# Kernel optimization log

Measured on AMD Instinct MI355X. Metric: run time of the kernel, lower is better.

## Reference

```python
import jax, jax.numpy as jnp
import numpy as np

N, LATENT, HIDDEN, OUT, B = 65536, 128, 512, 64, 1024
W_WIDTH = 4.0  # LSH bucket width params['w']


def setup_inputs() -> dict:
    key = jax.random.key(0)
    ks = jax.random.split(key, 6)
    return {
        "z": jax.random.normal(ks[0], (N, LATENT), jnp.float32),
        "W1": jax.random.normal(ks[1], (LATENT, HIDDEN), jnp.float32) / np.float32(np.sqrt(LATENT)),
        "b1": jnp.zeros((HIDDEN,), jnp.float32),
        "W2": jax.random.normal(ks[2], (HIDDEN, OUT), jnp.float32) / np.float32(np.sqrt(HIDDEN)),
        "b2": jnp.zeros((OUT,), jnp.float32),
        "a": jax.random.normal(ks[3], (OUT,), jnp.float32),
        "lsh_b": jax.random.uniform(ks[4], (1,), jnp.float32) * W_WIDTH,
    }


def reference(z, W1, b1, W2, b2, a, lsh_b):
    # decoder MLP: latent -> hidden (relu) -> output_dim
    h = jax.nn.relu(z @ W1 + b1)
    x = h @ W2 + b2                                     # [N, OUT]
    # LSH random-projection hash: floor((x.a + b)/w), bucketed mod B
    code = jnp.floor((x @ a + lsh_b[0]) / W_WIDTH)
    bucket = jnp.mod(code.astype(jnp.int32), B)         # [N] segment ids
    # dict-based cluster grouping -> segmented mean per hash bucket
    sums = jax.ops.segment_sum(x, bucket, num_segments=B)                # [B, OUT]
    counts = jax.ops.segment_sum(jnp.ones((x.shape[0],), x.dtype), bucket, num_segments=B)
    means = sums / jnp.maximum(counts, 1.0)[:, None]    # [B, OUT]
    # squared distances point -> every cluster mean (gram trick, no [N,B,OUT] tensor)
    d2 = jnp.maximum(
        jnp.sum(x * x, -1)[:, None] + jnp.sum(means * means, -1)[None, :]
        - 2.0 * (x @ means.T),
        0.0)                                            # [N, B]
    # DEC-style Student-t soft cluster assignment
    q = 1.0 / (1.0 + d2)
    q_s = q / jnp.sum(q, -1, keepdims=True)
    return (q_s, means)
```

## Files before the change

### kernel.cpp

```cpp
#include <hip/hip_runtime.h>
#include <hip/hip_bf16.h>

#define N_PTS   65536
#define LATENT  128
#define HIDDEN  512
#define OUT_D   64
#define NBUCKET 1024
#define ROWS_A  32

typedef __attribute__((ext_vector_type(8))) short frag_ab;
typedef __attribute__((ext_vector_type(4))) float f32x4;

__device__ __forceinline__ short bf16h(float f) {
    union { float f; unsigned u; } c; c.f = f;
    const unsigned r = (c.u + 0x7FFFu + ((c.u >> 16) & 1u)) >> 16;
    return (short)r;
}
__device__ __forceinline__ float bf16tof(short s) {
    union { unsigned u; float f; } c; c.u = ((unsigned)(unsigned short)s) << 16;
    return c.f;
}

__global__ __launch_bounds__(256) void prep_weights(
    const float* __restrict__ W1, const float* __restrict__ W2,
    short* __restrict__ w1frag, short* __restrict__ w2frag)
{
    const int tid = blockIdx.x * 256 + threadIdx.x;
    if (tid < 32 * 64 * 4) {
        const int ct = tid >> 8, l = (tid >> 2) & 63, ks = tid & 3;
        const int n = ct * 16 + (l & 15);
        const int k0 = ks * 32 + ((l >> 4) << 3);
        frag_ab hi, lo;
#pragma unroll
        for (int e = 0; e < 8; ++e) {
            const float wv = W1[(size_t)(k0 + e) * HIDDEN + n];
            const short h = bf16h(wv);
            hi[e] = h;
            lo[e] = bf16h(wv - bf16tof(h));
        }
        frag_ab* dst = (frag_ab*)w1frag;
        const int u = ((ct * 64 + l) * 4 + ks) * 2;
        dst[u] = hi; dst[u + 1] = lo;
    } else {
        const int u0 = tid - 32 * 64 * 4;
        const int c = u0 >> 8, ot = (u0 >> 6) & 3, l = u0 & 63;
        const int n = ot * 16 + (l & 15);
        const int k0 = c * 32 + ((l >> 4) << 3);
        frag_ab hi, lo;
#pragma unroll
        for (int e = 0; e < 8; ++e) {
            const float wv = W2[(size_t)(k0 + e) * OUT_D + n];
            const short h = bf16h(wv);
            hi[e] = h;
            lo[e] = bf16h(wv - bf16tof(h));
        }
        frag_ab* dst = (frag_ab*)w2frag;
        const int u = ((c * 4 + ot) * 64 + l) * 2;
        dst[u] = hi; dst[u + 1] = lo;
    }
}

#define WB_UNITS 1728
#define W2_OFF   1152
#define H_OFF    3456
#define HW_UNITS 320
#define XP_STRIDE 512
#define BAND_U   5e-4f

__global__ __launch_bounds__(256, 2) void mlp_mfma_kernel(
    const float* __restrict__ z, const short* __restrict__ w1frag,
    const short* __restrict__ w2frag, const float* __restrict__ b1,
    const float* __restrict__ b2, const float* __restrict__ a,
    const float* __restrict__ lsh_b,
    short* __restrict__ xhi, short* __restrict__ xlo,
    float* __restrict__ xnorm_out, int* __restrict__ bucket_out,
    int* __restrict__ wsflag)
{
    __shared__ frag_ab LD[H_OFF + 4 * HW_UNITS];
    short* LDs = (short*)LD;
    const int t = threadIdx.x;
    const int l = t & 63, w = t >> 6;
    const int row0 = blockIdx.x * 128 + w * 32;

    frag_ab zh[2][4], zl[2][4];
#pragma unroll
    for (int rt = 0; rt < 2; ++rt)
#pragma unroll
        for (int ks = 0; ks < 4; ++ks) {
            const float* src = z + (size_t)(row0 + rt * 16 + (l & 15)) * LATENT
                             + ks * 32 + ((l >> 4) << 3);
            const float4 p0 = *(const float4*)src;
            const float4 p1 = *(const float4*)(src + 4);
            const float v[8] = {p0.x, p0.y, p0.z, p0.w, p1.x, p1.y, p1.z, p1.w};
#pragma unroll
            for (int e = 0; e < 8; ++e) {
                const short h = bf16h(v[e]);
                zh[rt][ks][e] = h;
                zl[rt][ks][e] = bf16h(v[e] - bf16tof(h));
            }
        }

    f32x4 acc2[2][4];
#pragma unroll
    for (int rt = 0; rt < 2; ++rt)
#pragma unroll
        for (int ot = 0; ot < 4; ++ot) acc2[rt][ot] = (f32x4){0.f, 0.f, 0.f, 0.f};

    const frag_ab* w1g = (const frag_ab*)w1frag;
    const frag_ab* w2g = (const frag_ab*)w2frag;
    const int hbase = H_OFF + w * HW_UNITS;

#pragma unroll
    for (int j = 0; j < 4; ++j) {
        const int i = t + 256 * j;
        LD[(i >> 9) * 576 + ((i >> 3) & 63) * 9 + (i & 7)] = w1g[i];
    }
#pragma unroll
    for (int j = 0; j < 2; ++j) {
        const int i = t + 256 * j;
        LD[W2_OFF + ((i >> 1) & 63) * 9 + (((i >> 7) << 1) | (i & 1))] = w2g[i];
    }
    __syncthreads();

#pragma unroll 1
    for (int c = 0; c < 16; ++c) {
        const int pb = (c & 1) * WB_UNITS;
        const int sb = WB_UNITS - pb;
        frag_ab st1[4], st2[2];
        if (c < 15) {
#pragma unroll
            for (int j = 0; j < 4; ++j) st1[j] = w1g[(c + 1) * 1024 + t + 256 * j];
#pragma unroll
            for (int j = 0; j < 2; ++j) st2[j] = w2g[(c + 1) * 512 + t + 256 * j];
        }
#pragma unroll
        for (int ct_l = 0; ct_l < 2; ++ct_l) {
            frag_ab bh[4], bl[4];
#pragma unroll
            for (int ks = 0; ks < 4; ++ks) {
                bh[ks] = LD[pb + ct_l * 576 + l * 9 + ks * 2];
                bl[ks] = LD[pb + ct_l * 576 + l * 9 + ks * 2 + 1];
            }
            const float b1v = b1[(c * 2 + ct_l) * 16 + (l & 15)];
            const int k_l = ct_l * 16 + (l & 15);
            const int gu = k_l >> 3, eu = k_l & 7;
#pragma unroll
            for (int rt = 0; rt < 2; ++rt) {
                f32x4 acc = (f32x4){0.f, 0.f, 0.f, 0.f};
#pragma unroll
                for (int ks = 0; ks < 4; ++ks) {
                    acc = __builtin_amdgcn_mfma_f32_16x16x32_bf16(zh[rt][ks], bh[ks], acc, 0, 0, 0);
                    acc = __builtin_amdgcn_mfma_f32_16x16x32_bf16(zh[rt][ks], bl[ks], acc, 0, 0, 0);
                    acc = __builtin_amdgcn_mfma_f32_16x16x32_bf16(zl[rt][ks], bh[ks], acc, 0, 0, 0);
                }
#pragma unroll
                for (int r = 0; r < 4; ++r) {
                    const float hv = fmaxf(acc[r] + b1v, 0.f);
                    const short hh = bf16h(hv);
                    const short hlo = bf16h(hv - bf16tof(hh));
                    const int row_l = rt * 16 + (l >> 4) * 4 + r;
                    LDs[(hbase + row_l * 5 + gu) * 8 + eu] = hh;
                    LDs[(hbase + 160 + row_l * 5 + gu) * 8 + eu] = hlo;
                }
            }
        }
        frag_ab ah[2], al[2];
#pragma unroll
        for (int rt = 0; rt < 2; ++rt) {
            const int row = rt * 16 + (l & 15);
            const int g = l >> 4;
            ah[rt] = LD[hbase + row * 5 + g];
            al[rt] = LD[hbase + 160 + row * 5 + g];
        }
#pragma unroll
        for (int ot = 0; ot < 4; ++ot) {
            const frag_ab b2h = LD[pb + W2_OFF + l * 9 + ot * 2];
            const frag_ab b2l = LD[pb + W2_OFF + l * 9 + ot * 2 + 1];
#pragma unroll
            for (int rt = 0; rt < 2; ++rt) {
                acc2[rt][ot] = __builtin_amdgcn_mfma_f32_16x16x32_bf16(ah[rt], b2h, acc2[rt][ot], 0, 0, 0);
                acc2[rt][ot] = __builtin_amdgcn_mfma_f32_16x16x32_bf16(ah[rt], b2l, acc2[rt][ot], 0, 0, 0);
                acc2[rt][ot] = __builtin_amdgcn_mfma_f32_16x16x32_bf16(al[rt], b2h, acc2[rt][ot], 0, 0, 0);
            }
        }
        if (c < 15) {
#pragma unroll
            for (int j = 0; j < 4; ++j) {
                const int i = t + 256 * j;
                LD[sb + (i >> 9) * 576 + ((i >> 3) & 63) * 9 + (i & 7)] = st1[j];
            }
#pragma unroll
            for (int j = 0; j < 2; ++j) {
                const int i = t + 256 * j;
                LD[sb + W2_OFF + ((i >> 1) & 63) * 9 + (((i >> 7) << 1) | (i & 1))] = st2[j];
            }
        }
        __syncthreads();
    }

    float b2v[4], av[4];
#pragma unroll
    for (int ot = 0; ot < 4; ++ot) {
        b2v[ot] = b2[ot * 16 + (l & 15)];
        av[ot]  = a[ot * 16 + (l & 15)];
    }
    const int pbase = w * XP_STRIDE;
    int flagged = 0;
    const float lb = lsh_b[0];
#pragma unroll
    for (int rt = 0; rt < 2; ++rt)
#pragma unroll
        for (int r = 0; r < 4; ++r) {
            float sp = 0.f, np = 0.f;
            const int row_l = rt * 16 + (l >> 4) * 4 + r;
#pragma unroll
            for (int ot = 0; ot < 4; ++ot) {
                const float xv = acc2[rt][ot][r] + b2v[ot];
                sp = fmaf(xv, av[ot], sp);
                np = fmaf(xv, xv, np);
                const int col = ot * 16 + (l & 15);
                const short xh = bf16h(xv);
                LDs[(pbase + row_l * 8 + (col >> 3)) * 8 + (col & 7)] = xh;
                LDs[(pbase + 256 + row_l * 8 + (col >> 3)) * 8 + (col & 7)] = bf16h(xv - bf16tof(xh));
            }
#pragma unroll
            for (int off = 8; off >= 1; off >>= 1) {
                sp += __shfl_xor(sp, off, 16);
                np += __shfl_xor(np, off, 16);
            }
            if ((l & 15) == 0) {
                const int row = row0 + row_l;
                const float v = sp + lb;
                const float u = v * 0.25f;
                const float fl = floorf(u);
                bucket_out[row] = ((int)fl) & (NBUCKET - 1);
                xnorm_out[row] = np;
                const float fr = u - fl;
                if (fr < BAND_U || fr > 1.f - BAND_U) flagged = 1;
            }
        }
    const unsigned long long fb = __ballot(flagged != 0);
    if (l == 0) wsflag[blockIdx.x * 4 + w] = (fb != 0ull) ? 1 : 0;

    frag_ab* xhi8 = (frag_ab*)xhi;
    frag_ab* xlo8 = (frag_ab*)xlo;
#pragma unroll
    for (int j = 0; j < 4; ++j) {
        const int u = l + 64 * j;
        const size_t gidx = (size_t)(row0 + (u >> 3)) * 8 + (u & 7);
        xhi8[gidx] = LD[pbase + u];
        xlo8[gidx] = LD[pbase + 256 + u];
    }
}

__global__ __launch_bounds__(256, 3) void mlp_fixup_kernel(
    const float* __restrict__ z, const float* __restrict__ W1,
    const float* __restrict__ b1, const float* __restrict__ W2,
    const float* __restrict__ b2, const float* __restrict__ a,
    const float* __restrict__ lsh_b, const int* __restrict__ wsflag,
    short* __restrict__ xhi, short* __restrict__ xlo,
    float* __restrict__ xnorm_out, int* __restrict__ bucket_out)
{
    if (wsflag[blockIdx.x] == 0) return;
    __shared__ float zt[ROWS_A][LATENT];
    __shared__ float ht[ROWS_A][256];
    const int t = threadIdx.x;
    const int row0 = blockIdx.x * ROWS_A;

    {
        const float4* z4 = reinterpret_cast<const float4*>(z + (size_t)row0 * LATENT);
        float4* zt4 = reinterpret_cast<float4*>(&zt[0][0]);
#pragma unroll
        for (int i = 0; i < 4; ++i) zt4[t + 256 * i] = z4[t + 256 * i];
    }
    __syncthreads();

    const int tx = t & 63, ty = t >> 6;
    const int txq = t & 31, tyq = t >> 5;

    float acc2[4][2];
#pragma unroll
    for (int i = 0; i < 4; ++i) { acc2[i][0] = 0.f; acc2[i][1] = 0.f; }

    for (int h = 0; h < 2; ++h) {
        float acc1[8][4];
#pragma unroll
        for (int i = 0; i < 8; ++i)
#pragma unroll
            for (int cc = 0; cc < 4; ++cc) acc1[i][cc] = 0.f;

        const int jbase = h * 256 + tx;
#pragma unroll 2
        for (int k = 0; k < LATENT; k += 4) {
            float wv[4][4];
#pragma unroll
            for (int kk = 0; kk < 4; ++kk)
#pragma unroll
                for (int cc = 0; cc < 4; ++cc)
                    wv[kk][cc] = W1[(size_t)(k + kk) * HIDDEN + jbase + 64 * cc];
            float4 zv[8];
#pragma unroll
            for (int i = 0; i < 8; ++i)
                zv[i] = *reinterpret_cast<const float4*>(&zt[ty * 8 + i][k]);
#pragma unroll
            for (int i = 0; i < 8; ++i)
#pragma unroll
                for (int cc = 0; cc < 4; ++cc) {
                    acc1[i][cc] = fmaf(zv[i].x, wv[0][cc], acc1[i][cc]);
                    acc1[i][cc] = fmaf(zv[i].y, wv[1][cc], acc1[i][cc]);
                    acc1[i][cc] = fmaf(zv[i].z, wv[2][cc], acc1[i][cc]);
                    acc1[i][cc] = fmaf(zv[i].w, wv[3][cc], acc1[i][cc]);
                }
        }
        float bb[4];
#pragma unroll
        for (int cc = 0; cc < 4; ++cc) bb[cc] = b1[jbase + 64 * cc];
#pragma unroll
        for (int i = 0; i < 8; ++i)
#pragma unroll
            for (int cc = 0; cc < 4; ++cc)
                ht[ty * 8 + i][tx + 64 * cc] = fmaxf(acc1[i][cc] + bb[cc], 0.f);
        __syncthreads();

#pragma unroll 2
        for (int k = 0; k < 256; k += 4) {
            float w2v[4][2];
#pragma unroll
            for (int kk = 0; kk < 4; ++kk) {
                w2v[kk][0] = W2[(size_t)(h * 256 + k + kk) * OUT_D + txq];
                w2v[kk][1] = W2[(size_t)(h * 256 + k + kk) * OUT_D + txq + 32];
            }
            float4 hv[4];
#pragma unroll
            for (int i = 0; i < 4; ++i)
                hv[i] = *reinterpret_cast<const float4*>(&ht[tyq * 4 + i][k]);
#pragma unroll
            for (int i = 0; i < 4; ++i)
#pragma unroll
                for (int cc = 0; cc < 2; ++cc) {
                    acc2[i][cc] = fmaf(hv[i].x, w2v[0][cc], acc2[i][cc]);
                    acc2[i][cc] = fmaf(hv[i].y, w2v[1][cc], acc2[i][cc]);
                    acc2[i][cc] = fmaf(hv[i].z, w2v[2][cc], acc2[i][cc]);
                    acc2[i][cc] = fmaf(hv[i].w, w2v[3][cc], acc2[i][cc]);
                }
        }
        __syncthreads();
    }

    const float bb0 = b2[txq], bb1 = b2[txq + 32];
    const float a0 = a[txq], a1 = a[txq + 32];
    const float lb = lsh_b[0];
#pragma unroll
    for (int i = 0; i < 4; ++i) {
        const int row = row0 + tyq * 4 + i;
        const float x0 = acc2[i][0] + bb0;
        const float x1 = acc2[i][1] + bb1;
        const short h0 = bf16h(x0), h1 = bf16h(x1);
        xhi[(size_t)row * OUT_D + txq]      = h0;
        xhi[(size_t)row * OUT_D + txq + 32] = h1;
        xlo[(size_t)row * OUT_D + txq]      = bf16h(x0 - bf16tof(h0));
        xlo[(size_t)row * OUT_D + txq + 32] = bf16h(x1 - bf16tof(h1));

        float sa = fmaf(x0, a0, x1 * a1);
        float sn = fmaf(x0, x0, x1 * x1);
#pragma unroll
        for (int off = 16; off >= 1; off >>= 1) {
            sa += __shfl_xor(sa, off, 32);
            sn += __shfl_xor(sn, off, 32);
        }
        if (txq == 0) {
            const float code = floorf((sa + lb) * 0.25f);
            bucket_out[row] = ((int)code) & (NBUCKET - 1);
            xnorm_out[row] = sn;
        }
    }
}

__global__ __launch_bounds__(256) void hist_kernel(
    const int* __restrict__ bucket, int* __restrict__ blockhist)
{
    __shared__ int h[NBUCKET];
    const int t = threadIdx.x, blk = blockIdx.x;
    for (int i = t; i < NBUCKET; i += 256) h[i] = 0;
    __syncthreads();
    const int rbase = blk * 1024;
#pragma unroll
    for (int i = 0; i < 4; ++i)
        atomicAdd(&h[bucket[rbase + i * 256 + t]], 1);
    __syncthreads();
    for (int i = t; i < NBUCKET; i += 256)
        blockhist[blk * NBUCKET + i] = h[i];
}

__global__ __launch_bounds__(1024) void scan_kernel(
    const int* __restrict__ blockhist, int* __restrict__ base,
    int* __restrict__ blockbase)
{
    __shared__ int sc[NBUCKET];
    const int b = threadIdx.x;
    int c = 0;
    for (int blk = 0; blk < 64; ++blk) c += blockhist[blk * NBUCKET + b];
    sc[b] = c;
    __syncthreads();
    for (int off = 1; off < NBUCKET; off <<= 1) {
        const int add = (b >= off) ? sc[b - off] : 0;
        __syncthreads();
        sc[b] += add;
        __syncthreads();
    }
    const int offset = sc[b] - c;
    base[b] = offset;
    if (b == NBUCKET - 1) base[NBUCKET] = offset + c;
    int run = offset;
    for (int blk = 0; blk < 64; ++blk) {
        blockbase[blk * NBUCKET + b] = run;
        run += blockhist[blk * NBUCKET + b];
    }
}

__global__ __launch_bounds__(256) void scatter_kernel(
    const int* __restrict__ bucket, const int* __restrict__ blockbase,
    int* __restrict__ order)
{
    __shared__ int lcur[NBUCKET];
    const int t = threadIdx.x, blk = blockIdx.x;
    for (int i = t; i < NBUCKET; i += 256) lcur[i] = 0;
    __syncthreads();
    const int rbase = blk * 1024;
#pragma unroll
    for (int i = 0; i < 4; ++i) {
        const int row = rbase + i * 256 + t;
        const int bk = bucket[row];
        const int r = atomicAdd(&lcur[bk], 1);
        order[blockbase[blk * NBUCKET + bk] + r] = row;
    }
}

__global__ __launch_bounds__(256) void chunksum_kernel(
    const short* __restrict__ xhi, const short* __restrict__ xlo,
    const int* __restrict__ order, const int* __restrict__ bucket,
    float* __restrict__ sums)
{
    const int t = threadIdx.x, lane = t & 63, w = t >> 6;
    const int c = blockIdx.x * 4 + w;
    const int i0 = c * 64;
    const int ordv = order[i0 + lane];
    const int bktv = bucket[ordv];
    float acc = 0.f;
    int cur = __shfl(bktv, 0, 64);
#pragma unroll 8
    for (int j = 0; j < 64; ++j) {
        const int rb = __shfl(ordv, j, 64);
        const int bb = __shfl(bktv, j, 64);
        if (bb != cur) {
            atomicAdd(&sums[(size_t)cur * OUT_D + lane], acc);
            acc = 0.f; cur = bb;
        }
        acc += bf16tof(xhi[(size_t)rb * OUT_D + lane])
             + bf16tof(xlo[(size_t)rb * OUT_D + lane]);
    }
    atomicAdd(&sums[(size_t)cur * OUT_D + lane], acc);
}

__global__ __launch_bounds__(64) void means_kernel(
    const float* __restrict__ sums, const int* __restrict__ base,
    float* __restrict__ means_out, float* __restrict__ mnorm,
    short* __restrict__ bfrag)
{
    const int b = blockIdx.x;
    const int k = threadIdx.x;
    const int cnt = base[b + 1] - base[b];
    const float m = sums[b * OUT_D + k] / fmaxf((float)cnt, 1.0f);
    means_out[b * OUT_D + k] = m;

    const short mh = bf16h(m);
    const short ml = bf16h(m - bf16tof(mh));
    const int tile = b >> 4, col = b & 15;
    const int lane = ((k & 31) >> 3) * 16 + col;
    const int f = (k >> 5) * 2;
    const size_t idx = ((size_t)(tile * 64 + lane) * 4 + f) * 8 + (k & 7);
    bfrag[idx] = mh;
    bfrag[idx + 8] = ml;

    float s = m * m;
#pragma unroll
    for (int off = 32; off >= 1; off >>= 1) s += __shfl_xor(s, off, 64);
    if (k == 0) mnorm[b] = s;
}

__global__ __launch_bounds__(256) void q_kernel(
    const short* __restrict__ xhi, const short* __restrict__ xlo,
    const float* __restrict__ xnorm, const short* __restrict__ bfrag,
    const float* __restrict__ mnorm, float* __restrict__ q_out)
{
    __shared__ float rs_lds[4][16];
    const int t = threadIdx.x;
    const int l = t & 63;
    const int w = t >> 6;
    const int row0 = blockIdx.x * 16;
    const int lrow = (l >> 4) * 4;
    const int lcol = l & 15;

    const frag_ab* xh8 = reinterpret_cast<const frag_ab*>(xhi);
    const frag_ab* xl8 = reinterpret_cast<const frag_ab*>(xlo);
    frag_ab ah[2], al[2];
#pragma unroll
    for (int kh = 0; kh < 2; ++kh) {
        const size_t idx8 = (size_t)(row0 + lcol) * 8 + kh * 4 + (l >> 4);
        ah[kh] = xh8[idx8];
        al[kh] = xl8[idx8];
    }

    float xn[4];
#pragma unroll
    for (int r = 0; r < 4; ++r) xn[r] = xnorm[row0 + lrow + r];

    const frag_ab* bf8 = reinterpret_cast<const frag_ab*>(bfrag);
    float qs[16][4];
    float rsp[4] = {0.f, 0.f, 0.f, 0.f};

#pragma unroll
    for (int j = 0; j < 16; ++j) {
        const int bt = w + 4 * j;
        const size_t bb = (size_t)(bt * 64 + l) * 4;
        const frag_ab b0h = bf8[bb + 0];
        const frag_ab b0l = bf8[bb + 1];
        const frag_ab b1h = bf8[bb + 2];
        const frag_ab b1l = bf8[bb + 3];

        f32x4 acc = {0.f, 0.f, 0.f, 0.f};
        acc = __builtin_amdgcn_mfma_f32_16x16x32_bf16(ah[0], b0h, acc, 0, 0, 0);
        acc = __builtin_amdgcn_mfma_f32_16x16x32_bf16(ah[1], b1h, acc, 0, 0, 0);
        acc = __builtin_amdgcn_mfma_f32_16x16x32_bf16(ah[0], b0l, acc, 0, 0, 0);
        acc = __builtin_amdgcn_mfma_f32_16x16x32_bf16(ah[1], b1l, acc, 0, 0, 0);
        acc = __builtin_amdgcn_mfma_f32_16x16x32_bf16(al[0], b0h, acc, 0, 0, 0);
        acc = __builtin_amdgcn_mfma_f32_16x16x32_bf16(al[1], b1h, acc, 0, 0, 0);

        const float mn = mnorm[bt * 16 + lcol];
#pragma unroll
        for (int r = 0; r < 4; ++r) {
            const float d2 = fmaxf(fmaf(-2.f, acc[r], xn[r] + mn), 0.f);
            const float qq = __builtin_amdgcn_rcpf(1.f + d2);
            qs[j][r] = qq;
            rsp[r] += qq;
        }
    }

#pragma unroll
    for (int off = 8; off >= 1; off >>= 1)
#pragma unroll
        for (int r = 0; r < 4; ++r) rsp[r] += __shfl_xor(rsp[r], off, 16);
    if (lcol == 0) {
#pragma unroll
        for (int r = 0; r < 4; ++r) rs_lds[w][lrow + r] = rsp[r];
    }
    __syncthreads();

    float inv[4];
#pragma unroll
    for (int r = 0; r < 4; ++r) {
        const float tot = rs_lds[0][lrow + r] + rs_lds[1][lrow + r]
                        + rs_lds[2][lrow + r] + rs_lds[3][lrow + r];
        inv[r] = __builtin_amdgcn_rcpf(tot);
    }

#pragma unroll
    for (int j = 0; j < 16; ++j) {
        const int col = (w + 4 * j) * 16 + lcol;
#pragma unroll
        for (int r = 0; r < 4; ++r)
            q_out[(size_t)(row0 + lrow + r) * NBUCKET + col] = qs[j][r] * inv[r];
    }
}

extern "C" void kernel_launch(void* const* d_in, const int* in_sizes, int n_in,
                              void* d_out, int out_size, void* d_ws, size_t ws_size,
                              hipStream_t stream) {
    const float* z    = (const float*)d_in[0];
    const float* W1   = (const float*)d_in[1];
    const float* b1   = (const float*)d_in[2];
    const float* W2   = (const float*)d_in[3];
    const float* b2   = (const float*)d_in[4];
    const float* a    = (const float*)d_in[5];
    const float* lshb = (const float*)d_in[6];

    float* q_out     = (float*)d_out;
    float* means_out = q_out + (size_t)N_PTS * NBUCKET;

    char* ws = (char*)d_ws;
    short* xhi    = (short*)ws;
    short* xlo    = xhi + (size_t)N_PTS * OUT_D;
    short* bfrag  = xlo + (size_t)N_PTS * OUT_D;
    short* w1frag = bfrag + (size_t)64 * 64 * 4 * 8;
    short* w2frag = w1frag + (size_t)32 * 64 * 8 * 8;
    float* xnorm  = (float*)(w2frag + (size_t)16 * 4 * 64 * 2 * 8);
    float* mnorm  = xnorm + N_PTS;
    float* sums   = mnorm + NBUCKET;
    int*   bucket = (int*)(sums + (size_t)NBUCKET * OUT_D);
    int*   order  = bucket + N_PTS;
    int*   blockhist = order + N_PTS;
    int*   blockbase = blockhist + 64 * NBUCKET;
    int*   base      = blockbase + 64 * NBUCKET;
    int*   wsflag    = base + NBUCKET + 1;

    hipMemsetAsync(sums, 0, (size_t)NBUCKET * OUT_D * sizeof(float), stream);

    prep_weights<<<48, 256, 0, stream>>>(W1, W2, w1frag, w2frag);
    mlp_mfma_kernel<<<N_PTS / 128, 256, 0, stream>>>(z, w1frag, w2frag, b1, b2, a, lshb,
                                                     xhi, xlo, xnorm, bucket, wsflag);
    mlp_fixup_kernel<<<N_PTS / ROWS_A, 256, 0, stream>>>(z, W1, b1, W2, b2, a, lshb, wsflag,
                                                         xhi, xlo, xnorm, bucket);
    hist_kernel<<<64, 256, 0, stream>>>(bucket, blockhist);
    scan_kernel<<<1, 1024, 0, stream>>>(blockhist, base, blockbase);
    scatter_kernel<<<64, 256, 0, stream>>>(bucket, blockbase, order);
    chunksum_kernel<<<256, 256, 0, stream>>>(xhi, xlo, order, bucket, sums);
    means_kernel<<<NBUCKET, 64, 0, stream>>>(sums, base, means_out, mnorm, bfrag);
    q_kernel<<<N_PTS / 16, 256, 0, stream>>>(xhi, xlo, xnorm, bfrag, mnorm, q_out);
}
```

Measured before the change: 257.0 us.

## Single-buffer MLP weight LDS, fold sums memset, widen q_kernel tile with bf16 staging

Result: slower. 286.4 us (+11.4%).

```diff
diff --git a/kernel.cpp b/kernel.cpp
--- a/kernel.cpp
+++ b/kernel.cpp
@@ -19,6 +19,9 @@
 __device__ __forceinline__ float bf16tof(short s) {
     union { unsigned u; float f; } c; c.u = ((unsigned)(unsigned short)s) << 16;
     return c.f;
+}
+__device__ __forceinline__ float fbits(unsigned u) {
+    union { unsigned u; float f; } c; c.u = u; return c.f;
 }
 
 __global__ __launch_bounds__(256) void prep_weights(
@@ -62,12 +65,12 @@
 
 #define WB_UNITS 1728
 #define W2_OFF   1152
-#define H_OFF    3456
+#define H_OFF    1728
 #define HW_UNITS 320
 #define XP_STRIDE 512
 #define BAND_U   5e-4f
 
-__global__ __launch_bounds__(256, 2) void mlp_mfma_kernel(
+__global__ __launch_bounds__(256, 3) void mlp_mfma_kernel(
     const float* __restrict__ z, const short* __restrict__ w1frag,
     const short* __restrict__ w2frag, const float* __restrict__ b1,
     const float* __restrict__ b2, const float* __restrict__ a,
@@ -81,6 +84,7 @@
     const int t = threadIdx.x;
     const int l = t & 63, w = t >> 6;
     const int row0 = blockIdx.x * 128 + w * 32;
+    const int hbase = H_OFF + w * HW_UNITS;
 
     frag_ab zh[2][4], zl[2][4];
 #pragma unroll
@@ -108,7 +112,6 @@
 
     const frag_ab* w1g = (const frag_ab*)w1frag;
     const frag_ab* w2g = (const frag_ab*)w2frag;
-    const int hbase = H_OFF + w * HW_UNITS;
 
 #pragma unroll
     for (int j = 0; j < 4; ++j) {
@@ -124,8 +127,6 @@
 
 #pragma unroll 1
     for (int c = 0; c < 16; ++c) {
-        const int pb = (c & 1) * WB_UNITS;
-        const int sb = WB_UNITS - pb;
         frag_ab st1[4], st2[2];
         if (c < 15) {
 #pragma unroll
@@ -138,8 +139,8 @@
             frag_ab bh[4], bl[4];
 #pragma unroll
             for (int ks = 0; ks < 4; ++ks) {
-                bh[ks] = LD[pb + ct_l * 576 + l * 9 + ks * 2];
-                bl[ks] = LD[pb + ct_l * 576 + l * 9 + ks * 2 + 1];
+                bh[ks] = LD[ct_l * 576 + l * 9 + ks * 2];
+                bl[ks] = LD[ct_l * 576 + l * 9 + ks * 2 + 1];
             }
             const float b1v = b1[(c * 2 + ct_l) * 16 + (l & 15)];
             const int k_l = ct_l * 16 + (l & 15);
@@ -174,8 +175,8 @@
         }
 #pragma unroll
         for (int ot = 0; ot < 4; ++ot) {
-            const frag_ab b2h = LD[pb + W2_OFF + l * 9 + ot * 2];
-            const frag_ab b2l = LD[pb + W2_OFF + l * 9 + ot * 2 + 1];
+            const frag_ab b2h = LD[W2_OFF + l * 9 + ot * 2];
+            const frag_ab b2l = LD[W2_OFF + l * 9 + ot * 2 + 1];
 #pragma unroll
             for (int rt = 0; rt < 2; ++rt) {
                 acc2[rt][ot] = __builtin_amdgcn_mfma_f32_16x16x32_bf16(ah[rt], b2h, acc2[rt][ot], 0, 0, 0);
@@ -183,19 +184,20 @@
                 acc2[rt][ot] = __builtin_amdgcn_mfma_f32_16x16x32_bf16(al[rt], b2h, acc2[rt][ot], 0, 0, 0);
             }
         }
+        __syncthreads();
         if (c < 15) {
 #pragma unroll
             for (int j = 0; j < 4; ++j) {
                 const int i = t + 256 * j;
-                LD[sb + (i >> 9) * 576 + ((i >> 3) & 63) * 9 + (i & 7)] = st1[j];
+                LD[(i >> 9) * 576 + ((i >> 3) & 63) * 9 + (i & 7)] = st1[j];
             }
 #pragma unroll
             for (int j = 0; j < 2; ++j) {
                 const int i = t + 256 * j;
-                LD[sb + W2_OFF + ((i >> 1) & 63) * 9 + (((i >> 7) << 1) | (i & 1))] = st2[j];
-            }
-        }
-        __syncthreads();
+                LD[W2_OFF + ((i >> 1) & 63) * 9 + (((i >> 7) << 1) | (i & 1))] = st2[j];
+            }
+            __syncthreads();
+        }
     }
 
     float b2v[4], av[4];
@@ -377,11 +379,13 @@
 }
 
 __global__ __launch_bounds__(256) void hist_kernel(
-    const int* __restrict__ bucket, int* __restrict__ blockhist)
+    const int* __restrict__ bucket, int* __restrict__ blockhist,
+    float* __restrict__ sums)
 {
     __shared__ int h[NBUCKET];
     const int t = threadIdx.x, blk = blockIdx.x;
     for (int i = t; i < NBUCKET; i += 256) h[i] = 0;
+    for (int i = t; i < NBUCKET; i += 256) sums[blk * NBUCKET + i] = 0.f;
     __syncthreads();
     const int rbase = blk * 1024;
 #pragma unroll
@@ -488,36 +492,40 @@
     if (k == 0) mnorm[b] = s;
 }
 
-__global__ __launch_bounds__(256) void q_kernel(
+__global__ __launch_bounds__(256, 3) void q_kernel(
     const short* __restrict__ xhi, const short* __restrict__ xlo,
     const float* __restrict__ xnorm, const short* __restrict__ bfrag,
     const float* __restrict__ mnorm, float* __restrict__ q_out)
 {
-    __shared__ float rs_lds[4][16];
+    __shared__ float rs_lds[4][2][16];
     const int t = threadIdx.x;
     const int l = t & 63;
     const int w = t >> 6;
-    const int row0 = blockIdx.x * 16;
+    const int row0 = blockIdx.x * 32;
     const int lrow = (l >> 4) * 4;
     const int lcol = l & 15;
 
     const frag_ab* xh8 = reinterpret_cast<const frag_ab*>(xhi);
     const frag_ab* xl8 = reinterpret_cast<const frag_ab*>(xlo);
-    frag_ab ah[2], al[2];
-#pragma unroll
-    for (int kh = 0; kh < 2; ++kh) {
-        const size_t idx8 = (size_t)(row0 + lcol) * 8 + kh * 4 + (l >> 4);
-        ah[kh] = xh8[idx8];
-        al[kh] = xl8[idx8];
-    }
-
-    float xn[4];
-#pragma unroll
-    for (int r = 0; r < 4; ++r) xn[r] = xnorm[row0 + lrow + r];
+    frag_ab ah[2][2], al[2][2];
+#pragma unroll
+    for (int s = 0; s < 2; ++s)
+#pragma unroll
+        for (int kh = 0; kh < 2; ++kh) {
+            const size_t idx8 = (size_t)(row0 + s * 16 + lcol) * 8 + kh * 4 + (l >> 4);
+            ah[s][kh] = xh8[idx8];
+            al[s][kh] = xl8[idx8];
+        }
+
+    float xn[2][4];
+#pragma unroll
+    for (int s = 0; s < 2; ++s)
+#pragma unroll
+        for (int r = 0; r < 4; ++r) xn[s][r] = xnorm[row0 + s * 16 + lrow + r];
 
     const frag_ab* bf8 = reinterpret_cast<const frag_ab*>(bfrag);
-    float qs[16][4];
-    float rsp[4] = {0.f, 0.f, 0.f, 0.f};
+    unsigned qp[2][16][2];
+    float rsp[2][4] = {{0.f,0.f,0.f,0.f},{0.f,0.f,0.f,0.f}};
 
 #pragma unroll
     for (int j = 0; j < 16; ++j) {
@@ -527,49 +535,72 @@
         const frag_ab b0l = bf8[bb + 1];
         const frag_ab b1h = bf8[bb + 2];
         const frag_ab b1l = bf8[bb + 3];
-
-        f32x4 acc = {0.f, 0.f, 0.f, 0.f};
-        acc = __builtin_amdgcn_mfma_f32_16x16x32_bf16(ah[0], b0h, acc, 0, 0, 0);
-        acc = __builtin_amdgcn_mfma_f32_16x16x32_bf16(ah[1], b1h, acc, 0, 0, 0);
-        acc = __builtin_amdgcn_mfma_f32_16x16x32_bf16(ah[0], b0l, acc, 0, 0, 0);
-        acc = __builtin_amdgcn_mfma_f32_16x16x32_bf16(ah[1], b1l, acc, 0, 0, 0);
-        acc = __builtin_amdgcn_mfma_f32_16x16x32_bf16(al[0], b0h, acc, 0, 0, 0);
-        acc = __builtin_amdgcn_mfma_f32_16x16x32_bf16(al[1], b1h, acc, 0, 0, 0);
-
         const float mn = mnorm[bt * 16 + lcol];
+
+#pragma unroll
+        for (int s = 0; s < 2; ++s) {
+            f32x4 acc = {0.f, 0.f, 0.f, 0.f};
+            acc = __builtin_amdgcn_mfma_f32_16x16x32_bf16(ah[s][0], b0h, acc, 0, 0, 0);
+            acc = __builtin_amdgcn_mfma_f32_16x16x32_bf16(ah[s][1], b1h, acc, 0, 0, 0);
+            acc = __builtin_amdgcn_mfma_f32_16x16x32_bf16(ah[s][0], b0l, acc, 0, 0, 0);
+            acc = __builtin_amdgcn_mfma_f32_16x16x32_bf16(ah[s][1], b1l, acc, 0, 0, 0);
+            acc = __builtin_amdgcn_mfma_f32_16x16x32_bf16(al[s][0], b0h, acc, 0, 0, 0);
+            acc = __builtin_amdgcn_mfma_f32_16x16x32_bf16(al[s][1], b1h, acc, 0, 0, 0);
+
+            float qq[4];
+#pragma unroll
+            for (int r = 0; r < 4; ++r) {
+                const float d2 = fmaxf(fmaf(-2.f, acc[r], xn[s][r] + mn), 0.f);
+                qq[r] = __builtin_amdgcn_rcpf(1.f + d2);
+                rsp[s][r] += qq[r];
+            }
+            qp[s][j][0] = ((unsigned)(unsigned short)bf16h(qq[1]) << 16)
+                        | (unsigned)(unsigned short)bf16h(qq[0]);
+            qp[s][j][1] = ((unsigned)(unsigned short)bf16h(qq[3]) << 16)
+                        | (unsigned)(unsigned short)bf16h(qq[2]);
+        }
+    }
+
+#pragma unroll
+    for (int off = 8; off >= 1; off >>= 1)
+#pragma unroll
+        for (int s = 0; s < 2; ++s)
+#pragma unroll
+            for (int r = 0; r < 4; ++r) rsp[s][r] += __shfl_xor(rsp[s][r], off, 16);
+    if (lcol == 0) {
+#pragma unroll
+        for (int s = 0; s < 2; ++s)
+#pragma unroll
+            for (int r = 0; r < 4; ++r) rs_lds[w][s][lrow + r] = rsp[s][r];
+    }
+    __syncthreads();
+
+    float inv[2][4];
+#pragma unroll
+    for (int s = 0; s < 2; ++s)
 #pragma unroll
         for (int r = 0; r < 4; ++r) {
-            const float d2 = fmaxf(fmaf(-2.f, acc[r], xn[r] + mn), 0.f);
-            const float qq = __builtin_amdgcn_rcpf(1.f + d2);
-            qs[j][r] = qq;
-            rsp[r] += qq;
-        }
-    }
-
-#pragma unroll
-    for (int off = 8; off >= 1; off >>= 1)
-#pragma unroll
-        for (int r = 0; r < 4; ++r) rsp[r] += __shfl_xor(rsp[r], off, 16);
-    if (lcol == 0) {
-#pragma unroll
-        for (int r = 0; r < 4; ++r) rs_lds[w][lrow + r] = rsp[r];
-    }
-    __syncthreads();
-
-    float inv[4];
-#pragma unroll
-    for (int r = 0; r < 4; ++r) {
-        const float tot = rs_lds[0][lrow + r] + rs_lds[1][lrow + r]
-                        + rs_lds[2][lrow + r] + rs_lds[3][lrow + r];
-        inv[r] = __builtin_amdgcn_rcpf(tot);
-    }
+            const float tot = rs_lds[0][s][lrow + r] + rs_lds[1][s][lrow + r]
+                            + rs_lds[2][s][lrow + r] + rs_lds[3][s][lrow + r];
+            inv[s][r] = __builtin_amdgcn_rcpf(tot);
+        }
 
 #pragma unroll
     for (int j = 0; j < 16; ++j) {
         const int col = (w + 4 * j) * 16 + lcol;
 #pragma unroll
-        for (int r = 0; r < 4; ++r)
-            q_out[(size_t)(row0 + lrow + r) * NBUCKET + col] = qs[j][r] * inv[r];
+        for (int s = 0; s < 2; ++s) {
+            const unsigned u0 = qp[s][j][0], u1 = qp[s][j][1];
+            const float q0 = fbits(u0 << 16);
+            const float q1 = fbits(u0 & 0xFFFF0000u);
+            const float q2 = fbits(u1 << 16);
+            const float q3 = fbits(u1 & 0xFFFF0000u);
+            const size_t rb = (size_t)(row0 + s * 16 + lrow) * NBUCKET + col;
+            q_out[rb]               = q0 * inv[s][0];
+            q_out[rb + NBUCKET]     = q1 * inv[s][1];
+            q_out[rb + 2 * NBUCKET] = q2 * inv[s][2];
+            q_out[rb + 3 * NBUCKET] = q3 * inv[s][3];
+        }
     }
 }
 
@@ -603,17 +634,15 @@
     int*   base      = blockbase + 64 * NBUCKET;
     int*   wsflag    = base + NBUCKET + 1;
 
-    hipMemsetAsync(sums, 0, (size_t)NBUCKET * OUT_D * sizeof(float), stream);
-
     prep_weights<<<48, 256, 0, stream>>>(W1, W2, w1frag, w2frag);
     mlp_mfma_kernel<<<N_PTS / 128, 256, 0, stream>>>(z, w1frag, w2frag, b1, b2, a, lshb,
                                                      xhi, xlo, xnorm, bucket, wsflag);
     mlp_fixup_kernel<<<N_PTS / ROWS_A, 256, 0, stream>>>(z, W1, b1, W2, b2, a, lshb, wsflag,
                                                          xhi, xlo, xnorm, bucket);
-    hist_kernel<<<64, 256, 0, stream>>>(bucket, blockhist);
+    hist_kernel<<<64, 256, 0, stream>>>(bucket, blockhist, sums);
     scan_kernel<<<1, 1024, 0, stream>>>(blockhist, base, blockbase);
     scatter_kernel<<<64, 256, 0, stream>>>(bucket, blockbase, order);
     chunksum_kernel<<<256, 256, 0, stream>>>(xhi, xlo, order, bucket, sums);
     means_kernel<<<NBUCKET, 64, 0, stream>>>(sums, base, means_out, mnorm, bfrag);
-    q_kernel<<<N_PTS / 16, 256, 0, stream>>>(xhi, xlo, xnorm, bfrag, mnorm, q_out);
-}
+    q_kernel<<<N_PTS / 32, 256, 0, stream>>>(xhi, xlo, xnorm, bfrag, mnorm, q_out);
+}
```
